# Kernel tuning notes

Hardware: AMD Instinct MI355X
Metric: run time of the kernel (lower is better)

## Reference

```python
import jax, jax.numpy as jnp
import numpy as np

NC = 128      # nc
K = 5         # cube kernel size
NS = 3        # n_scale pyramid levels
NV = 150000   # vertices (cortical-surface scale)
NF = 300000   # faces ~ 2*NV
L = 192       # volume side (L = W = H -> rescale = [1,1,1])


def setup_inputs() -> dict:
    key = jax.random.key(0)
    ks = jax.random.split(key, 16)
    s = 0.05
    return {
        "v": jax.random.uniform(ks[0], (1, NV, 3), minval=-0.9, maxval=0.9, dtype=jnp.float32),
        "f": jax.random.randint(ks[1], (1, NF, 3), 0, NV, dtype=jnp.int32),
        "volume": jax.random.normal(ks[2], (1, 1, L, L, L), dtype=jnp.float32),
        "fc1_w": jax.random.normal(ks[3], (6, NC), dtype=jnp.float32) * s,
        "fc1_b": jnp.zeros((NC,), jnp.float32),
        "fc2_w": jax.random.normal(ks[4], (2 * NC, 4 * NC), dtype=jnp.float32) * s,
        "fc2_b": jnp.zeros((4 * NC,), jnp.float32),
        "fc3_w": jax.random.normal(ks[5], (4 * NC, 2 * NC), dtype=jnp.float32) * s,
        "fc3_b": jnp.zeros((2 * NC,), jnp.float32),
        "fc4_w": jax.random.normal(ks[6], (2 * NC, 3), dtype=jnp.float32) * s,
        "fc4_b": jnp.zeros((3,), jnp.float32),
        "conv_w": jax.random.normal(ks[7], (NC, NS, K, K, K), dtype=jnp.float32) * s,
        "conv_b": jnp.zeros((NC,), jnp.float32),
        "lfc_w": jax.random.normal(ks[8], (NC, NC), dtype=jnp.float32) * s,
        "lfc_b": jnp.zeros((NC,), jnp.float32),
    }


def _vertex_normals(v, f):
    # pytorch3d-style vertex normals: scatter-add area-weighted face normals, then normalize.
    verts, faces = v[0], f[0]
    p0, p1, p2 = verts[faces[:, 0]], verts[faces[:, 1]], verts[faces[:, 2]]
    fn = jnp.cross(p1 - p0, p2 - p0)  # [NF, 3]
    n = jnp.zeros_like(verts)
    n = n.at[faces[:, 0]].add(fn).at[faces[:, 1]].add(fn).at[faces[:, 2]].add(fn)
    n = n / jnp.maximum(jnp.linalg.norm(n, axis=-1, keepdims=True), 1e-12)
    return n[None]  # [1, NV, 3]


def _cube_sampling(v, volume):
    # Vectorized version of the 125-iteration Python gather loop:
    # gather a KxKxK neighborhood per vertex at each pyramid scale.
    vol_n = volume[0, 0]
    off = jnp.arange(-(K - 1) // 2, (K - 1) // 2 + 1)  # [-2..2]
    cubes = []
    for n in range(NS):
        if n > 0:
            s = vol_n.shape[0]
            vol_n = vol_n.reshape(s // 2, 2, s // 2, 2, s // 2, 2).mean(axis=(1, 3, 5))  # avg_pool3d(2)
        idx = jnp.round((v[0] + 1.0) * L / 2 ** (n + 1)).astype(jnp.int32)  # rescale = [1,1,1]
        idx = jnp.clip(idx, (K - 1) // 2, L // 2 ** n - 3)
        i0 = idx[:, 0, None, None, None] + off[None, :, None, None]
        i1 = idx[:, 1, None, None, None] + off[None, None, :, None]
        i2 = idx[:, 2, None, None, None] + off[None, None, None, :]
        cubes.append(vol_n[i0, i1, i2])  # [NV, K, K, K]
    return jnp.stack(cubes, axis=1)  # [NV, NS, K, K, K]


def reference(v, f, volume, fc1_w, fc1_b, fc2_w, fc2_b, fc3_w, fc3_b, fc4_w, fc4_b,
              conv_w, conv_b, lfc_w, lfc_b):
    coord = v
    normal = _vertex_normals(v, f)
    x = jnp.concatenate([v, normal], axis=2)                 # [1, NV, 6]
    x = jax.nn.leaky_relu(x @ fc1_w + fc1_b, 0.15)           # [1, NV, NC]
    cubes = _cube_sampling(v, volume)                        # [NV, NS, K, K, K]
    # Conv3d with kernel == input size -> single output voxel == full contraction.
    x_local = jnp.einsum('ncijk,ocijk->no', cubes, conv_w) + conv_b  # [NV, NC]
    x_local = (x_local @ lfc_w + lfc_b)[None]                # [1, NV, NC]
    x = jnp.concatenate([x, x_local], axis=2)                # [1, NV, 2*NC]
    x = jax.nn.leaky_relu(x @ fc2_w + fc2_b, 0.15)
    x = jax.nn.leaky_relu(x @ fc3_w + fc3_b, 0.15)
    x = jnp.tanh(x @ fc4_w + fc4_b) * 0.1
    return coord + x
```

## Files before the change

kernel.cpp:

```cpp
#include <hip/hip_runtime.h>
#include <hip/hip_bf16.h>
#include <math.h>

#define NVERT 150000
#define NFACE 300000
#define LVOL  192
#define TVB   32
#define MTV   48

#define P2_POOL1 3456
#define P2_POOL2 432
#define P2_WC    193
#define P2_WC8   304
#define P2_CP0   3456
#define P2_POOL2_START (P2_POOL1)
#define P2_WC_START    (P2_POOL1 + P2_POOL2)
#define P2_WC8_START   (P2_WC_START + P2_WC)
#define P2_CP0_START   (P2_WC8_START + P2_WC8)

#define NB_NORM 1172
#define NB_TRS  1024

#define NBUCKET 13824
#define WS_BIG_NEED  44808576ull
#define WS_B16_NEED  58964352ull
#define WS_SORT_NEED 60219648ull

typedef short v8s __attribute__((ext_vector_type(8)));
typedef float v4f __attribute__((ext_vector_type(4)));
typedef unsigned int v4u __attribute__((ext_vector_type(4)));

__device__ __forceinline__ float s2f(short s) {
    unsigned int u = ((unsigned int)(unsigned short)s) << 16;
    return __builtin_bit_cast(float, u);
}
__device__ __forceinline__ short f2s(float f) {
    __hip_bfloat16 h = __float2bfloat16(f);
    return __builtin_bit_cast(short, h);
}
__device__ __forceinline__ float lrelu(float x) { return x > 0.f ? x : 0.15f * x; }

__device__ __forceinline__ float ldf(const void* __restrict__ p, int i, int bf) {
    return bf ? s2f(((const short*)p)[i]) : ((const float*)p)[i];
}

__device__ __forceinline__ int haddr(int r, int c) {
    int hi  = c >> 7;
    int mid = (c >> 4) & 7;
    int lo  = c & 15;
    int wc  = hi * 64 + (mid & 3) * 16 + lo;
    return ((mid < 4) ? 0 : 12672) + r * 264 + wc;
}

__global__ void detect_kernel(const void* __restrict__ v, int* __restrict__ flag) {
    __shared__ int s_ok;
    int t = threadIdx.x;
    if (t == 0) s_ok = 1;
    __syncthreads();
    float x = s2f(((const short*)v)[t]);
    if (!(fabsf(x) <= 1.0f)) atomicAnd(&s_ok, 0);
    __syncthreads();
    if (t == 0) *flag = s_ok;
}

__global__ __launch_bounds__(256) void sort_hist_kernel(
    const void* __restrict__ v, int* __restrict__ hist, int* __restrict__ keys,
    const int* __restrict__ flag)
{
    const int bf = *flag;
    int vert = blockIdx.x * 256 + threadIdx.x;
    if (vert >= NVERT) return;
    float vx = ldf(v, vert * 3 + 0, bf);
    float vy = ldf(v, vert * 3 + 1, bf);
    float vz = ldf(v, vert * 3 + 2, bf);
    int cx = min(max((int)rintf((vx + 1.0f) * 96.0f), 2), 189);
    int cy = min(max((int)rintf((vy + 1.0f) * 96.0f), 2), 189);
    int cz = min(max((int)rintf((vz + 1.0f) * 96.0f), 2), 189);
    int key = ((cx >> 3) * 24 + (cy >> 3)) * 24 + (cz >> 3);
    keys[vert] = key;
    atomicAdd(&hist[key], 1);
}

__global__ __launch_bounds__(1024) void sort_scan_kernel(int* __restrict__ hist)
{
    __shared__ int partial[1024];
    const int t = threadIdx.x;
    const int CH = 14;
    int base = t * CH;
    int sum = 0;
    #pragma unroll
    for (int i = 0; i < CH; i++) {
        int idx = base + i;
        if (idx < NBUCKET) sum += hist[idx];
    }
    partial[t] = sum;
    __syncthreads();
    for (int off = 1; off < 1024; off <<= 1) {
        int x = (t >= off) ? partial[t - off] : 0;
        __syncthreads();
        partial[t] += x;
        __syncthreads();
    }
    int run = partial[t] - sum;
    for (int i = 0; i < CH; i++) {
        int idx = base + i;
        if (idx < NBUCKET) {
            int c = hist[idx];
            hist[idx] = run;
            run += c;
        }
    }
}

__global__ __launch_bounds__(256) void sort_scatter_kernel(
    int* __restrict__ cursor, const int* __restrict__ keys, int* __restrict__ perm)
{
    int vert = blockIdx.x * 256 + threadIdx.x;
    if (vert >= NVERT) return;
    int pos = atomicAdd(&cursor[keys[vert]], 1);
    perm[pos] = vert;
}

__global__ __launch_bounds__(256) void mega_prep2_kernel(
    const void* __restrict__ volume,
    short* __restrict__ vol1b, short* __restrict__ vol2b,
    const void* __restrict__ conv_w, const void* __restrict__ lfc_w,
    const void* __restrict__ conv_b, const void* __restrict__ lfc_b,
    short* __restrict__ Wcomb, short* __restrict__ Wcomb8, float* __restrict__ bcomb,
    const int* __restrict__ flag,
    short* __restrict__ vol0b)
{
    const int bf = *flag;
    const int bid = blockIdx.x;
    const int t = threadIdx.x;

    if (bid < P2_POOL1) {
        int id = bid * 256 + t;
        int z = id % 96, y = (id / 96) % 96, x = id / (96 * 96);
        float s = 0.f;
        #pragma unroll
        for (int a = 0; a < 2; a++)
            #pragma unroll
            for (int b = 0; b < 2; b++)
                #pragma unroll
                for (int c = 0; c < 2; c++)
                    s += ldf(volume, (2 * x + a) * (LVOL * LVOL) + (2 * y + b) * LVOL + (2 * z + c), bf);
        s *= 0.125f;
        vol1b[id] = f2s(s);
    } else if (bid < P2_WC_START) {
        int id = (bid - P2_POOL2_START) * 256 + t;
        int z = id % 48, y = (id / 48) % 48, x = id / (48 * 48);
        float s = 0.f;
        for (int a = 0; a < 4; a++)
            for (int b = 0; b < 4; b++)
                #pragma unroll
                for (int c = 0; c < 4; c++)
                    s += ldf(volume, (4 * x + a) * (LVOL * LVOL) + (4 * y + b) * LVOL + (4 * z + c), bf);
        s *= 0.015625f;
        vol2b[id] = f2s(s);
    } else if (bid < P2_WC8_START) {
        int id = (bid - P2_WC_START) * 256 + t;
        if (id < 49152) {
            int j = id / 384, k = id - j * 384;
            float acc = 0.f;
            if (k < 375) {
                float a0 = 0.f, a1 = 0.f, a2 = 0.f, a3 = 0.f;
                for (int o = 0; o < 128; o += 4) {
                    a0 += ldf(conv_w, (o + 0) * 375 + k, bf) * ldf(lfc_w, (o + 0) * 128 + j, bf);
                    a1 += ldf(conv_w, (o + 1) * 375 + k, bf) * ldf(lfc_w, (o + 1) * 128 + j, bf);
                    a2 += ldf(conv_w, (o + 2) * 375 + k, bf) * ldf(lfc_w, (o + 2) * 128 + j, bf);
                    a3 += ldf(conv_w, (o + 3) * 375 + k, bf) * ldf(lfc_w, (o + 3) * 128 + j, bf);
                }
                acc = (a0 + a1) + (a2 + a3);
            }
            int tile = j >> 4, ln = j & 15;
            int kk = k >> 5, r = k & 31, qq = r >> 3, e = r & 7;
            Wcomb[((tile * 12 + kk) * 64 + qq * 16 + ln) * 8 + e] = f2s(acc);
        } else if (id < 49152 + 128) {
            int j = id - 49152;
            float acc = ldf(lfc_b, j, bf);
            for (int o = 0; o < 128; o++) acc += ldf(conv_b, o, bf) * ldf(lfc_w, o * 128 + j, bf);
            bcomb[j] = acc;
        }
    } else if (bid < P2_CP0_START) {
        int id = (bid - P2_WC8_START) * 256 + t;
        int j = id / 608, k = id - j * 608;
        int r = k >> 3, e = k & 7;
        float acc = 0.f;
        if (e < 5 && r < 75) {
            int k375 = (r / 25) * 125 + (r % 25) * 5 + e;
            float a0 = 0.f, a1 = 0.f, a2 = 0.f, a3 = 0.f;
            for (int o = 0; o < 128; o += 4) {
                a0 += ldf(conv_w, (o + 0) * 375 + k375, bf) * ldf(lfc_w, (o + 0) * 128 + j, bf);
                a1 += ldf(conv_w, (o + 1) * 375 + k375, bf) * ldf(lfc_w, (o + 1) * 128 + j, bf);
                a2 += ldf(conv_w, (o + 2) * 375 + k375, bf) * ldf(lfc_w, (o + 2) * 128 + j, bf);
                a3 += ldf(conv_w, (o + 3) * 375 + k375, bf) * ldf(lfc_w, (o + 3) * 128 + j, bf);
            }
            acc = (a0 + a1) + (a2 + a3);
        }
        int tile = j >> 4, ln = j & 15;
        int kk = k >> 5, rr = k & 31, qq = rr >> 3, ee = rr & 7;
        Wcomb8[((tile * 19 + kk) * 64 + qq * 16 + ln) * 8 + ee] = f2s(acc);
    } else {
        if (bf) return;
        int id = (bid - P2_CP0_START) * 2048 + t * 8;
        const float* vp = (const float*)volume;
        short tmp[8];
        #pragma unroll
        for (int i = 0; i < 8; i++) tmp[i] = f2s(vp[id + i]);
        *(v8s*)&vol0b[id] = *(v8s*)tmp;
    }
}

__global__ __launch_bounds__(256, 4) void gather8_kernel(
    const void* __restrict__ v,
    const int* __restrict__ f, float* __restrict__ n_accum,
    const void* __restrict__ volume,
    const short* __restrict__ vol1b,
    const short* __restrict__ vol2b,
    const short* __restrict__ vol0b,
    const int* __restrict__ perm,
    const short* __restrict__ Wcomb8,
    const float* __restrict__ bcomb,
    const void* __restrict__ fc2_w, const void* __restrict__ fc3_w,
    short* __restrict__ fc2T, short* __restrict__ fc3T,
    short* __restrict__ xloc,
    const int* __restrict__ flag, int ngather)
{
    __shared__ __align__(16) short sCube[TVB * 608];
    __shared__ int sIdx[TVB * 4];

    const int bf = *flag;
    const int t = threadIdx.x;
    const int bid = blockIdx.x;

    if (bid >= ngather) {
        int rb = bid - ngather;
        if (rb < NB_NORM) {
            int ft = rb * 256 + t;
            if (ft >= NFACE) return;
            int i0 = f[ft * 3 + 0], i1 = f[ft * 3 + 1], i2 = f[ft * 3 + 2];
            float p0x = ldf(v, i0 * 3 + 0, bf), p0y = ldf(v, i0 * 3 + 1, bf), p0z = ldf(v, i0 * 3 + 2, bf);
            float p1x = ldf(v, i1 * 3 + 0, bf), p1y = ldf(v, i1 * 3 + 1, bf), p1z = ldf(v, i1 * 3 + 2, bf);
            float p2x = ldf(v, i2 * 3 + 0, bf), p2y = ldf(v, i2 * 3 + 1, bf), p2z = ldf(v, i2 * 3 + 2, bf);
            float e1x = p1x - p0x, e1y = p1y - p0y, e1z = p1z - p0z;
            float e2x = p2x - p0x, e2y = p2y - p0y, e2z = p2z - p0z;
            float cx = e1y * e2z - e1z * e2y;
            float cy = e1z * e2x - e1x * e2z;
            float cz = e1x * e2y - e1y * e2x;
            atomicAdd(&n_accum[i0 * 3 + 0], cx); atomicAdd(&n_accum[i0 * 3 + 1], cy); atomicAdd(&n_accum[i0 * 3 + 2], cz);
            atomicAdd(&n_accum[i1 * 3 + 0], cx); atomicAdd(&n_accum[i1 * 3 + 1], cy); atomicAdd(&n_accum[i1 * 3 + 2], cz);
            atomicAdd(&n_accum[i2 * 3 + 0], cx); atomicAdd(&n_accum[i2 * 3 + 1], cy); atomicAdd(&n_accum[i2 * 3 + 2], cz);
        } else {
            int id = (rb - NB_NORM) * 256 + t;
            if (id < 131072) {
                int col = id >> 8, k = id & 255;
                int tile = col >> 4, ln = col & 15;
                int kk = k >> 5, r = k & 31, qq = r >> 3, e = r & 7;
                fc2T[((tile * 8 + kk) * 64 + qq * 16 + ln) * 8 + e] = f2s(ldf(fc2_w, k * 512 + col, bf));
            } else {
                int i = id - 131072;
                int col = i >> 9, k = i & 511;
                int tile = col >> 4, ln = col & 15;
                int kk = k >> 5, r = k & 31, qq = r >> 3, e = r & 7;
                fc3T[((tile * 16 + kk) * 64 + qq * 16 + ln) * 8 + e] = f2s(ldf(fc3_w, k * 256 + col, bf));
            }
        }
        return;
    }

    const int base = bid * TVB;
    const int w = t >> 6, L = t & 63, q = L >> 4, ln = L & 15;
    const short* v0 = bf ? (const short*)volume : vol0b;

    if (t < TVB) {
        int slot = min(base + t, NVERT - 1);
        int vert = perm ? perm[slot] : slot;
        float vx = ldf(v, vert * 3 + 0, bf);
        float vy = ldf(v, vert * 3 + 1, bf);
        float vz = ldf(v, vert * 3 + 2, bf);
        #pragma unroll
        for (int n = 0; n < 3; n++) {
            float scl = (n == 0) ? 96.0f : (n == 1 ? 48.0f : 24.0f);
            int dim = LVOL >> n, lim = dim - 3;
            int cx = min(max((int)rintf((vx + 1.0f) * scl), 2), lim);
            int cy = min(max((int)rintf((vy + 1.0f) * scl), 2), lim);
            int cz = min(max((int)rintf((vz + 1.0f) * scl), 2), lim);
            sIdx[t * 4 + n] = (cx * dim + cy) * dim + (cz - 2);
        }
        *(v4u*)&sCube[t * 608 + 600] = (v4u){0u, 0u, 0u, 0u};
    }
    __syncthreads();

    for (int idx = t; idx < TVB * 75; idx += 256) {
        int n   = idx / 800;
        int rem = idx - n * 800;
        int vl  = rem / 25;
        int dd  = rem - vl * 25;
        int di  = dd / 5, dj = dd - di * 5;
        int dim = LVOL >> n;
        int addr = sIdx[vl * 4 + n] + (di - 2) * dim * dim + (dj - 2) * dim;
        int r = n * 25 + dd;
        if (n == 0 && bf) {
            const short* vp = (const short*)volume;
            short* dst = &sCube[vl * 608 + r * 8];
            #pragma unroll
            for (int i = 0; i < 5; i++) dst[i] = vp[addr + i];
            dst[5] = 0; dst[6] = 0; dst[7] = 0;
        } else {
            const short* lvl = (n == 0) ? v0 : (n == 1 ? vol1b : vol2b);
            int p  = addr & 1;
            int a0 = addr - p;
            const unsigned int* u = (const unsigned int*)(lvl + a0);
            unsigned int x0 = u[0], x1 = u[1], x2 = u[2];
            unsigned int d0, d1, d2;
            if (p) {
                d0 = (x0 >> 16) | (x1 << 16);
                d1 = (x1 >> 16) | (x2 << 16);
                d2 = (x2 >> 16);
            } else {
                d0 = x0;
                d1 = x1;
                d2 = x2 & 0xFFFFu;
            }
            *(v4u*)&sCube[vl * 608 + r * 8] = (v4u){d0, d1, d2, 0u};
        }
    }
    __syncthreads();

    #pragma unroll
    for (int nt = 0; nt < 2; nt++) {
        int col = w * 32 + nt * 16 + ln;
        const short* wb = Wcomb8 + ((w * 2 + nt) * 19 * 64 + q * 16 + ln) * 8;
        v4f acc0 = {0.f, 0.f, 0.f, 0.f}, acc1 = {0.f, 0.f, 0.f, 0.f};
        #pragma unroll
        for (int k0 = 0; k0 < 19; k0++) {
            v8s b  = *(const v8s*)(wb + k0 * 512);
            v8s a0 = *(const v8s*)&sCube[ln * 608 + k0 * 32 + q * 8];
            v8s a1 = *(const v8s*)&sCube[(16 + ln) * 608 + k0 * 32 + q * 8];
            acc0 = __builtin_amdgcn_mfma_f32_16x16x32_bf16(a0, b, acc0, 0, 0, 0);
            acc1 = __builtin_amdgcn_mfma_f32_16x16x32_bf16(a1, b, acc1, 0, 0, 0);
        }
        float bias = bcomb[col];
        #pragma unroll
        for (int r = 0; r < 4; r++) {
            xloc[(base + q * 4 + r) * 128 + col]      = f2s(acc0[r] + bias);
            xloc[(base + 16 + q * 4 + r) * 128 + col] = f2s(acc1[r] + bias);
        }
    }
}

__global__ __launch_bounds__(256, 6) void gather_ext_kernel(
    const void* __restrict__ v,
    const int* __restrict__ f, float* __restrict__ n_accum,
    const void* __restrict__ volume,
    const short* __restrict__ vol1b,
    const short* __restrict__ vol2b,
    const short* __restrict__ vol0b,
    const int* __restrict__ perm,
    const short* __restrict__ Wcomb,
    const float* __restrict__ bcomb,
    const void* __restrict__ fc2_w, const void* __restrict__ fc3_w,
    short* __restrict__ fc2T, short* __restrict__ fc3T,
    short* __restrict__ xloc,
    const int* __restrict__ flag, int ngather)
{
    __shared__ __align__(16) short sCube[TVB * 392];
    __shared__ int sIdx[TVB * 4];

    const int bf = *flag;
    const int t = threadIdx.x;
    const int bid = blockIdx.x;

    if (bid >= ngather) {
        int rb = bid - ngather;
        if (rb < NB_NORM) {
            int ft = rb * 256 + t;
            if (ft >= NFACE) return;
            int i0 = f[ft * 3 + 0], i1 = f[ft * 3 + 1], i2 = f[ft * 3 + 2];
            float p0x = ldf(v, i0 * 3 + 0, bf), p0y = ldf(v, i0 * 3 + 1, bf), p0z = ldf(v, i0 * 3 + 2, bf);
            float p1x = ldf(v, i1 * 3 + 0, bf), p1y = ldf(v, i1 * 3 + 1, bf), p1z = ldf(v, i1 * 3 + 2, bf);
            float p2x = ldf(v, i2 * 3 + 0, bf), p2y = ldf(v, i2 * 3 + 1, bf), p2z = ldf(v, i2 * 3 + 2, bf);
            float e1x = p1x - p0x, e1y = p1y - p0y, e1z = p1z - p0z;
            float e2x = p2x - p0x, e2y = p2y - p0y, e2z = p2z - p0z;
            float cx = e1y * e2z - e1z * e2y;
            float cy = e1z * e2x - e1x * e2z;
            float cz = e1x * e2y - e1y * e2x;
            atomicAdd(&n_accum[i0 * 3 + 0], cx); atomicAdd(&n_accum[i0 * 3 + 1], cy); atomicAdd(&n_accum[i0 * 3 + 2], cz);
            atomicAdd(&n_accum[i1 * 3 + 0], cx); atomicAdd(&n_accum[i1 * 3 + 1], cy); atomicAdd(&n_accum[i1 * 3 + 2], cz);
            atomicAdd(&n_accum[i2 * 3 + 0], cx); atomicAdd(&n_accum[i2 * 3 + 1], cy); atomicAdd(&n_accum[i2 * 3 + 2], cz);
        } else {
            int id = (rb - NB_NORM) * 256 + t;
            if (id < 131072) {
                int col = id >> 8, k = id & 255;
                int tile = col >> 4, ln = col & 15;
                int kk = k >> 5, r = k & 31, qq = r >> 3, e = r & 7;
                fc2T[((tile * 8 + kk) * 64 + qq * 16 + ln) * 8 + e] = f2s(ldf(fc2_w, k * 512 + col, bf));
            } else {
                int i = id - 131072;
                int col = i >> 9, k = i & 511;
                int tile = col >> 4, ln = col & 15;
                int kk = k >> 5, r = k & 31, qq = r >> 3, e = r & 7;
                fc3T[((tile * 16 + kk) * 64 + qq * 16 + ln) * 8 + e] = f2s(ldf(fc3_w, k * 256 + col, bf));
            }
        }
        return;
    }

    const int base = bid * TVB;
    const int w = t >> 6, L = t & 63, q = L >> 4, ln = L & 15;
    const short* v0 = bf ? (const short*)volume : vol0b;

    if (t < TVB) {
        int slot = min(base + t, NVERT - 1);
        int vert = perm ? perm[slot] : slot;
        float vx = ldf(v, vert * 3 + 0, bf);
        float vy = ldf(v, vert * 3 + 1, bf);
        float vz = ldf(v, vert * 3 + 2, bf);
        #pragma unroll
        for (int n = 0; n < 3; n++) {
            float scl = (n == 0) ? 96.0f : (n == 1 ? 48.0f : 24.0f);
            int dim = LVOL >> n, lim = dim - 3;
            int cx = min(max((int)rintf((vx + 1.0f) * scl), 2), lim);
            int cy = min(max((int)rintf((vy + 1.0f) * scl), 2), lim);
            int cz = min(max((int)rintf((vz + 1.0f) * scl), 2), lim);
            sIdx[t * 4 + n] = (cx * dim + cy) * dim + (cz - 2);
        }
    }
    __syncthreads();

    for (int idx = t; idx < TVB * 75; idx += 256) {
        int n   = idx / 800;
        int rem = idx - n * 800;
        int vl  = rem / 25;
        int dd  = rem - vl * 25;
        int di  = dd / 5, dj = dd - di * 5;
        int dim = LVOL >> n;
        int addr = sIdx[vl * 4 + n] + (di - 2) * dim * dim + (dj - 2) * dim;
        short* dst = &sCube[vl * 392 + n * 125 + dd * 5];
        if (n == 0 && v0 == nullptr) {
            const float* vp = (const float*)volume;
            #pragma unroll
            for (int i = 0; i < 5; i++) dst[i] = f2s(vp[addr + i]);
        } else {
            const short* lvl = (n == 0) ? v0 : (n == 1 ? vol1b : vol2b);
            #pragma unroll
            for (int i = 0; i < 5; i++) dst[i] = lvl[addr + i];
        }
    }
    for (int idx = t; idx < TVB * 9; idx += 256) {
        int vl = idx / 9, rr = idx - vl * 9;
        sCube[vl * 392 + 375 + rr] = 0;
    }
    __syncthreads();

    #pragma unroll
    for (int nt = 0; nt < 2; nt++) {
        int col = w * 32 + nt * 16 + ln;
        const short* wb = Wcomb + ((w * 2 + nt) * 12 * 64 + q * 16 + ln) * 8;
        v4f acc0 = {0.f, 0.f, 0.f, 0.f}, acc1 = {0.f, 0.f, 0.f, 0.f};
        #pragma unroll
        for (int k0 = 0; k0 < 12; k0++) {
            v8s b  = *(const v8s*)(wb + k0 * 512);
            v8s a0 = *(const v8s*)&sCube[ln * 392 + k0 * 32 + q * 8];
            v8s a1 = *(const v8s*)&sCube[(16 + ln) * 392 + k0 * 32 + q * 8];
            acc0 = __builtin_amdgcn_mfma_f32_16x16x32_bf16(a0, b, acc0, 0, 0, 0);
            acc1 = __builtin_amdgcn_mfma_f32_16x16x32_bf16(a1, b, acc1, 0, 0, 0);
        }
        float bias = bcomb[col];
        #pragma unroll
        for (int r = 0; r < 4; r++) {
            xloc[(base + q * 4 + r) * 128 + col]      = f2s(acc0[r] + bias);
            xloc[(base + 16 + q * 4 + r) * 128 + col] = f2s(acc1[r] + bias);
        }
    }
}

__global__ __launch_bounds__(256, 3) void mlp_kernel(
    const void* __restrict__ v,
    const float* __restrict__ n_accum,
    const short* __restrict__ xloc,
    const int* __restrict__ perm,
    const short* __restrict__ fc2T,
    const short* __restrict__ fc3T,
    const void* __restrict__ fc1_w, const void* __restrict__ fc1_b,
    const void* __restrict__ fc2_b, const void* __restrict__ fc3_b,
    const void* __restrict__ fc4_w, const void* __restrict__ fc4_b,
    void* __restrict__ out,
    const int* __restrict__ flag)
{
    __shared__ __align__(16) char smem[52224];
    short* sX  = (short*)smem;
    short* sHB = (short*)smem;
    short* s3  = (short*)smem;
    short* sW4 = (short*)(smem + 50688);

    const int bf = *flag;
    const int t = threadIdx.x;
    const int base = blockIdx.x * MTV;
    const int w = t >> 6, L = t & 63, q = L >> 4, ln = L & 15;
    const int laneoff = (q * 16 + ln) * 8;

    for (int id = t; id < MTV * 16; id += 256) {
        int row = id >> 4, seg = id & 15;
        v8s x = *(const v8s*)(xloc + (base + row) * 128 + seg * 8);
        *(v8s*)&sX[row * 264 + 128 + seg * 8] = x;
    }

    for (int i = t; i < 768; i += 256) {
        int j = i >> 8, k = i & 255;
        sW4[i] = f2s(ldf(fc4_w, k * 3 + j, bf));
    }

    {
        int vi = t >> 2, cb = (t & 3) * 32;
        if (vi < MTV) {
            int vert = perm ? perm[base + vi] : (base + vi);
            float i0 = ldf(v, vert * 3 + 0, bf);
            float i1 = ldf(v, vert * 3 + 1, bf);
            float i2 = ldf(v, vert * 3 + 2, bf);
            float nx = n_accum[vert * 3 + 0];
            float ny = n_accum[vert * 3 + 1];
            float nz = n_accum[vert * 3 + 2];
            float inv = 1.0f / fmaxf(sqrtf(nx * nx + ny * ny + nz * nz), 1e-12f);
            float i3 = nx * inv, i4 = ny * inv, i5 = nz * inv;
            #pragma unroll 8
            for (int i = 0; i < 32; i++) {
                int c = cb + i;
                float acc = ldf(fc1_b, c, bf)
                          + i0 * ldf(fc1_w, 0 * 128 + c, bf)
                          + i1 * ldf(fc1_w, 1 * 128 + c, bf)
                          + i2 * ldf(fc1_w, 2 * 128 + c, bf)
                          + i3 * ldf(fc1_w, 3 * 128 + c, bf)
                          + i4 * ldf(fc1_w, 4 * 128 + c, bf)
                          + i5 * ldf(fc1_w, 5 * 128 + c, bf);
                sX[vi * 264 + c] = f2s(lrelu(acc));
            }
        }
    }
    __syncthreads();

    {
        #pragma unroll
        for (int nt = 4; nt < 8; nt++) {
            int col = w * 128 + nt * 16 + ln;
            const short* bb = fc2T + (w * 8 + nt) * 8 * 512 + laneoff;
            v4f acc0 = {0.f, 0.f, 0.f, 0.f}, acc1 = {0.f, 0.f, 0.f, 0.f}, acc2 = {0.f, 0.f, 0.f, 0.f};
            #pragma unroll
            for (int k0 = 0; k0 < 8; k0++) {
                v8s b  = *(const v8s*)(bb + k0 * 512);
                v8s a0 = *(const v8s*)&sX[(ln) * 264 + k0 * 32 + q * 8];
                v8s a1 = *(const v8s*)&sX[(16 + ln) * 264 + k0 * 32 + q * 8];
                v8s a2 = *(const v8s*)&sX[(32 + ln) * 264 + k0 * 32 + q * 8];
                acc0 = __builtin_amdgcn_mfma_f32_16x16x32_bf16(a0, b, acc0, 0, 0, 0);
                acc1 = __builtin_amdgcn_mfma_f32_16x16x32_bf16(a1, b, acc1, 0, 0, 0);
                acc2 = __builtin_amdgcn_mfma_f32_16x16x32_bf16(a2, b, acc2, 0, 0, 0);
            }
            float bias = ldf(fc2_b, col, bf);
            int wc = 12672 + w * 64 + (nt - 4) * 16 + ln;
            #pragma unroll
            for (int r = 0; r < 4; r++) {
                sHB[(q * 4 + r) * 264 + wc]      = f2s(lrelu(acc0[r] + bias));
                sHB[(16 + q * 4 + r) * 264 + wc] = f2s(lrelu(acc1[r] + bias));
                sHB[(32 + q * 4 + r) * 264 + wc] = f2s(lrelu(acc2[r] + bias));
            }
        }

        v4f accL[4][3];
        #pragma unroll
        for (int nt = 0; nt < 4; nt++)
            #pragma unroll
            for (int m = 0; m < 3; m++)
                accL[nt][m] = (v4f){0.f, 0.f, 0.f, 0.f};

        #pragma unroll
        for (int nt = 0; nt < 4; nt++) {
            const short* bb = fc2T + (w * 8 + nt) * 8 * 512 + laneoff;
            #pragma unroll
            for (int k0 = 0; k0 < 8; k0++) {
                v8s b  = *(const v8s*)(bb + k0 * 512);
                v8s a0 = *(const v8s*)&sX[(ln) * 264 + k0 * 32 + q * 8];
                v8s a1 = *(const v8s*)&sX[(16 + ln) * 264 + k0 * 32 + q * 8];
                v8s a2 = *(const v8s*)&sX[(32 + ln) * 264 + k0 * 32 + q * 8];
                accL[nt][0] = __builtin_amdgcn_mfma_f32_16x16x32_bf16(a0, b, accL[nt][0], 0, 0, 0);
                accL[nt][1] = __builtin_amdgcn_mfma_f32_16x16x32_bf16(a1, b, accL[nt][1], 0, 0, 0);
                accL[nt][2] = __builtin_amdgcn_mfma_f32_16x16x32_bf16(a2, b, accL[nt][2], 0, 0, 0);
            }
        }
        __syncthreads();

        #pragma unroll
        for (int nt = 0; nt < 4; nt++) {
            int col = w * 128 + nt * 16 + ln;
            float bias = ldf(fc2_b, col, bf);
            int wc = w * 64 + nt * 16 + ln;
            #pragma unroll
            for (int r = 0; r < 4; r++) {
                sHB[(q * 4 + r) * 264 + wc]      = f2s(lrelu(accL[nt][0][r] + bias));
                sHB[(16 + q * 4 + r) * 264 + wc] = f2s(lrelu(accL[nt][1][r] + bias));
                sHB[(32 + q * 4 + r) * 264 + wc] = f2s(lrelu(accL[nt][2][r] + bias));
            }
        }
    }
    __syncthreads();

    {
        v4f acc[4][3];
        #pragma unroll
        for (int nt = 0; nt < 4; nt++)
            #pragma unroll
            for (int m = 0; m < 3; m++)
                acc[nt][m] = (v4f){0.f, 0.f, 0.f, 0.f};

        #pragma unroll
        for (int half = 0; half < 2; half++) {
            v8s A0[8], A1[8], A2[8];
            #pragma unroll
            for (int k0 = 0; k0 < 8; k0++) {
                int c = half * 256 + k0 * 32 + q * 8;
                A0[k0] = *(const v8s*)&sHB[haddr(ln, c)];
                A1[k0] = *(const v8s*)&sHB[haddr(16 + ln, c)];
                A2[k0] = *(const v8s*)&sHB[haddr(32 + ln, c)];
            }
            #pragma unroll
            for (int nt = 0; nt < 4; nt++) {
                const short* bb = fc3T + ((w * 4 + nt) * 16 + half * 8) * 512 + laneoff;
                v8s B[8];
                #pragma unroll
                for (int k0 = 0; k0 < 8; k0++) B[k0] = *(const v8s*)(bb + k0 * 512);
                #pragma unroll
                for (int k0 = 0; k0 < 8; k0++) {
                    acc[nt][0] = __builtin_amdgcn_mfma_f32_16x16x32_bf16(A0[k0], B[k0], acc[nt][0], 0, 0, 0);
                    acc[nt][1] = __builtin_amdgcn_mfma_f32_16x16x32_bf16(A1[k0], B[k0], acc[nt][1], 0, 0, 0);
                    acc[nt][2] = __builtin_amdgcn_mfma_f32_16x16x32_bf16(A2[k0], B[k0], acc[nt][2], 0, 0, 0);
                }
            }
        }
        __syncthreads();

        #pragma unroll
        for (int nt = 0; nt < 4; nt++) {
            int col = w * 64 + nt * 16 + ln;
            float bias = ldf(fc3_b, col, bf);
            #pragma unroll
            for (int r = 0; r < 4; r++) {
                s3[(q * 4 + r) * 264 + col]      = f2s(lrelu(acc[nt][0][r] + bias));
                s3[(16 + q * 4 + r) * 264 + col] = f2s(lrelu(acc[nt][1][r] + bias));
                s3[(32 + q * 4 + r) * 264 + col] = f2s(lrelu(acc[nt][2][r] + bias));
            }
        }
    }
    __syncthreads();

    {
        int vi = t >> 2, l = t & 3;
        if (vi < MTV) {
            float p0 = 0.f, p1 = 0.f, p2 = 0.f;
            for (int k = l * 8; k < 256; k += 32) {
                #pragma unroll
                for (int j = 0; j < 8; j++) {
                    float a = s2f(s3[vi * 264 + k + j]);
                    p0 += a * s2f(sW4[0 * 256 + k + j]);
                    p1 += a * s2f(sW4[1 * 256 + k + j]);
                    p2 += a * s2f(sW4[2 * 256 + k + j]);
                }
            }
            #pragma unroll
            for (int s = 2; s; s >>= 1) {
                p0 += __shfl_down(p0, s, 4);
                p1 += __shfl_down(p1, s, 4);
                p2 += __shfl_down(p2, s, 4);
            }
            if (l == 0) {
                int vert = perm ? perm[base + vi] : (base + vi);
                float vx = ldf(v, vert * 3 + 0, bf);
                float vy = ldf(v, vert * 3 + 1, bf);
                float vz = ldf(v, vert * 3 + 2, bf);
                float o0 = vx + 0.1f * tanhf(p0 + ldf(fc4_b, 0, bf));
                float o1 = vy + 0.1f * tanhf(p1 + ldf(fc4_b, 1, bf));
                float o2 = vz + 0.1f * tanhf(p2 + ldf(fc4_b, 2, bf));
                if (bf) {
                    short* ob = (short*)out;
                    ob[vert * 3 + 0] = f2s(o0);
                    ob[vert * 3 + 1] = f2s(o1);
                    ob[vert * 3 + 2] = f2s(o2);
                } else {
                    float* of = (float*)out;
                    of[vert * 3 + 0] = o0;
                    of[vert * 3 + 1] = o1;
                    of[vert * 3 + 2] = o2;
                }
            }
        }
    }
}

__global__ __launch_bounds__(256, 3) void fused_mfma_kernel(
    const void* __restrict__ v,
    const float* __restrict__ n_accum,
    const void* __restrict__ volume,
    const short* __restrict__ vol1,
    const short* __restrict__ vol2,
    const short* __restrict__ Wcomb,
    const float* __restrict__ bcomb,
    const short* __restrict__ fc2T,
    const short* __restrict__ fc3T,
    const void* __restrict__ fc1_w, const void* __restrict__ fc1_b,
    const void* __restrict__ fc2_b, const void* __restrict__ fc3_b,
    const void* __restrict__ fc4_w, const void* __restrict__ fc4_b,
    void* __restrict__ out,
    const int* __restrict__ flag)
{
    __shared__ __align__(16) char smem[51712];
    short* sX    = (short*)smem;
    short* sCube = (short*)(smem + 16896);
    short* sH    = (short*)(smem + 16896);
    short* s3    = (short*)smem;
    short* sW4   = (short*)(smem + 50176);

    const int bf = *flag;
    const int t = threadIdx.x;
    const int base = blockIdx.x * TVB;
    const int w = t >> 6, L = t & 63, q = L >> 4, ln = L & 15;
    const int laneoff = (q * 16 + ln) * 8;

    for (int idx = t; idx < TVB * 75; idx += 256) {
        int vl  = idx / 75;
        int r75 = idx - vl * 75;
        int n   = r75 / 25;
        int dd  = r75 - n * 25;
        int di  = dd / 5, dj = dd - di * 5;
        int vert = base + vl;
        short* dst = &sCube[vl * 392 + n * 125 + dd * 5];
        if (vert < NVERT) {
            float vx = ldf(v, vert * 3 + 0, bf);
            float vy = ldf(v, vert * 3 + 1, bf);
            float vz = ldf(v, vert * 3 + 2, bf);
            float scl = (n == 0) ? 96.0f : (n == 1 ? 48.0f : 24.0f);
            int lim = (LVOL >> n) - 3;
            int cx = (int)rintf((vx + 1.0f) * scl);
            int cy = (int)rintf((vy + 1.0f) * scl);
            int cz = (int)rintf((vz + 1.0f) * scl);
            cx = min(max(cx, 2), lim) + di - 2;
            cy = min(max(cy, 2), lim) + dj - 2;
            cz = min(max(cz, 2), lim);
            if (n == 0) {
                int b0 = (cx * LVOL + cy) * LVOL + (cz - 2);
                if (bf) {
                    const short* vp = (const short*)volume;
                    #pragma unroll
                    for (int i = 0; i < 5; i++) dst[i] = vp[b0 + i];
                } else {
                    const float* vp = (const float*)volume;
                    #pragma unroll
                    for (int i = 0; i < 5; i++) dst[i] = f2s(vp[b0 + i]);
                }
            } else {
                const short* lvl = (n == 1) ? vol1 : vol2;
                int dim = (n == 1) ? 96 : 48;
                int b0 = (cx * dim + cy) * dim + (cz - 2);
// ... 118 lines not shown
        }
    }
    __syncthreads();

    {
        int vi = t >> 3, l = t & 7;
        float p0 = 0.f, p1 = 0.f, p2 = 0.f;
        for (int k = l; k < 256; k += 8) {
            float a = s2f(s3[vi * 264 + k]);
            p0 += a * s2f(sW4[0 * 256 + k]);
            p1 += a * s2f(sW4[1 * 256 + k]);
            p2 += a * s2f(sW4[2 * 256 + k]);
        }
        #pragma unroll
        for (int s = 4; s; s >>= 1) {
            p0 += __shfl_down(p0, s, 8);
            p1 += __shfl_down(p1, s, 8);
            p2 += __shfl_down(p2, s, 8);
        }
        if (l == 0) {
            int vert = base + vi;
            if (vert < NVERT) {
                float vx = ldf(v, vert * 3 + 0, bf);
                float vy = ldf(v, vert * 3 + 1, bf);
                float vz = ldf(v, vert * 3 + 2, bf);
                float o0 = vx + 0.1f * tanhf(p0 + ldf(fc4_b, 0, bf));
                float o1 = vy + 0.1f * tanhf(p1 + ldf(fc4_b, 1, bf));
                float o2 = vz + 0.1f * tanhf(p2 + ldf(fc4_b, 2, bf));
                if (bf) {
                    short* ob = (short*)out;
                    ob[vert * 3 + 0] = f2s(o0);
                    ob[vert * 3 + 1] = f2s(o1);
                    ob[vert * 3 + 2] = f2s(o2);
                } else {
                    float* of = (float*)out;
                    of[vert * 3 + 0] = o0;
                    of[vert * 3 + 1] = o1;
                    of[vert * 3 + 2] = o2;
                }
            }
        }
    }
}

extern "C" void kernel_launch(void* const* d_in, const int* in_sizes, int n_in,
                              void* d_out, int out_size, void* d_ws, size_t ws_size,
                              hipStream_t stream) {
    const void* v      = d_in[0];
    const int*  f      = (const int*)d_in[1];
    const void* volume = d_in[2];
    const void* fc1_w  = d_in[3];
    const void* fc1_b  = d_in[4];
    const void* fc2_w  = d_in[5];
    const void* fc2_b  = d_in[6];
    const void* fc3_w  = d_in[7];
    const void* fc3_b  = d_in[8];
    const void* fc4_w  = d_in[9];
    const void* fc4_b  = d_in[10];
    const void* conv_w = d_in[11];
    const void* conv_b = d_in[12];
    const void* lfc_w  = d_in[13];
    const void* lfc_b  = d_in[14];

    char* wsb = (char*)d_ws;
    const int big  = (ws_size >= WS_BIG_NEED) ? 1 : 0;
    const int b16  = (ws_size >= WS_B16_NEED) ? 1 : 0;
    const int srt  = (ws_size >= WS_SORT_NEED) ? 1 : 0;

    if (big) {
        int*   flag    = (int*)wsb;
        float* n_accum = (float*)(wsb + 64);
        short* vol1b   = (short*)(wsb + 1800064);
        short* vol2b   = (short*)(wsb + 5339008);
        short* Wcomb8  = (short*)(wsb + 5560192);
        short* Wcomb   = (short*)(wsb + 5781376);
        float* bcomb   = (float*)(wsb + 5879680);
        short* fc2T    = (short*)(wsb + 5880192);
        short* fc3T    = (short*)(wsb + 6142336);
        short* xloc    = (short*)(wsb + 6404480);
        short* vol0b   = b16 ? (short*)(wsb + 44808576) : nullptr;
        int*   hist    = srt ? (int*)(wsb + 58964352) : nullptr;
        int*   keys    = srt ? (int*)(wsb + 59019648) : nullptr;
        int*   perm    = srt ? (int*)(wsb + 59619648) : nullptr;

        hipMemsetAsync(n_accum, 0, NVERT * 3 * sizeof(float), stream);
        detect_kernel<<<1, 256, 0, stream>>>(v, flag);
        if (srt) {
            hipMemsetAsync(hist, 0, NBUCKET * sizeof(int), stream);
            sort_hist_kernel<<<(NVERT + 255) / 256, 256, 0, stream>>>(v, hist, keys, flag);
            sort_scan_kernel<<<1, 1024, 0, stream>>>(hist);
            sort_scatter_kernel<<<(NVERT + 255) / 256, 256, 0, stream>>>(hist, keys, perm);
        }
        mega_prep2_kernel<<<P2_CP0_START + (b16 ? P2_CP0 : 0), 256, 0, stream>>>(
            volume, vol1b, vol2b,
            conv_w, lfc_w, conv_b, lfc_b, Wcomb, Wcomb8, bcomb, flag, vol0b);
        int ngather = (NVERT + TVB - 1) / TVB;
        if (srt) {
            gather8_kernel<<<ngather + NB_NORM + NB_TRS, 256, 0, stream>>>(
                v, f, n_accum, volume, vol1b, vol2b, vol0b, perm, Wcomb8, bcomb,
                fc2_w, fc3_w, fc2T, fc3T, xloc, flag, ngather);
        } else {
            gather_ext_kernel<<<ngather + NB_NORM + NB_TRS, 256, 0, stream>>>(
                v, f, n_accum, volume, vol1b, vol2b, vol0b, nullptr, Wcomb, bcomb,
                fc2_w, fc3_w, fc2T, fc3T, xloc, flag, ngather);
        }
        mlp_kernel<<<(NVERT + MTV - 1) / MTV, 256, 0, stream>>>(
            v, n_accum, xloc, perm, fc2T, fc3T,
            fc1_w, fc1_b, fc2_b, fc3_b, fc4_w, fc4_b, d_out, flag);
    } else {
        int*   flag    = (int*)wsb;
        float* n_accum = (float*)(wsb + 64);
        short* vol1    = (short*)(wsb + 1800064);
        short* vol2    = (short*)(wsb + 3569536);
        short* Wcomb   = (short*)(wsb + 3790720);
        float* bcomb   = (float*)(wsb + 3889024);
        short* fc2T    = (short*)(wsb + 3889536);
        short* fc3T    = (short*)(wsb + 4151680);

        hipMemsetAsync(n_accum, 0, NVERT * 3 * sizeof(float), stream);
        detect_kernel<<<1, 256, 0, stream>>>(v, flag);
        mega_prep2_kernel<<<P2_WC8_START, 256, 0, stream>>>(
            volume, vol1, vol2,
            conv_w, lfc_w, conv_b, lfc_b, Wcomb, nullptr, bcomb, flag, nullptr);
        gather_ext_kernel<<<NB_NORM + NB_TRS, 256, 0, stream>>>(
            v, f, n_accum, volume, vol1, vol2, nullptr, nullptr, Wcomb, bcomb,
            fc2_w, fc3_w, fc2T, fc3T, nullptr, flag, 0);
        fused_mfma_kernel<<<(NVERT + TVB - 1) / TVB, 256, 0, stream>>>(
            v, n_accum, volume, vol1, vol2, Wcomb, bcomb, fc2T, fc3T,
            fc1_w, fc1_b, fc2_b, fc3_b, fc4_w, fc4_b, d_out, flag);
    }
}
```

Baseline: 550.6 us.

## Store sorted vertex coords and rank-indexed normals to avoid perm indirection

The sort scatter step now also writes each vertex's sorted position and a copy of its coordinates in sorted order. Face-normal atomics accumulate into the sorted slot via the rank array. The gather and MLP kernels can then read coordinates and normals contiguously by slot instead of going through perm. This removes scattered indirect loads in the hot kernels at the cost of extra workspace, an extra rank lookup per face vertex, and extra writes in the scatter kernel.

```diff
diff --git a/kernel.cpp b/kernel.cpp
--- a/kernel.cpp
+++ b/kernel.cpp
@@ -24,7 +24,7 @@
 #define NBUCKET 13824
 #define WS_BIG_NEED  44808576ull
 #define WS_B16_NEED  58964352ull
-#define WS_SORT_NEED 60219648ull
+#define WS_SORT_NEED 62619648ull
 
 typedef short v8s __attribute__((ext_vector_type(8)));
 typedef float v4f __attribute__((ext_vector_type(4)));
@@ -113,12 +113,20 @@
 }
 
 __global__ __launch_bounds__(256) void sort_scatter_kernel(
-    int* __restrict__ cursor, const int* __restrict__ keys, int* __restrict__ perm)
+    const void* __restrict__ v,
+    int* __restrict__ cursor, const int* __restrict__ keys,
+    int* __restrict__ perm, int* __restrict__ rank, float* __restrict__ vperm,
+    const int* __restrict__ flag)
 {
+    const int bf = *flag;
     int vert = blockIdx.x * 256 + threadIdx.x;
     if (vert >= NVERT) return;
     int pos = atomicAdd(&cursor[keys[vert]], 1);
     perm[pos] = vert;
+    rank[vert] = pos;
+    vperm[pos * 3 + 0] = ldf(v, vert * 3 + 0, bf);
+    vperm[pos * 3 + 1] = ldf(v, vert * 3 + 1, bf);
+    vperm[pos * 3 + 2] = ldf(v, vert * 3 + 2, bf);
 }
 
 __global__ __launch_bounds__(256) void mega_prep2_kernel(
@@ -219,7 +227,8 @@
     const short* __restrict__ vol1b,
     const short* __restrict__ vol2b,
     const short* __restrict__ vol0b,
-    const int* __restrict__ perm,
+    const float* __restrict__ vperm,
+    const int* __restrict__ rank,
     const short* __restrict__ Wcomb8,
     const float* __restrict__ bcomb,
     const void* __restrict__ fc2_w, const void* __restrict__ fc3_w,
@@ -228,6 +237,143 @@
     const int* __restrict__ flag, int ngather)
 {
     __shared__ __align__(16) short sCube[TVB * 608];
+    __shared__ int sIdx[TVB * 4];
+
+    const int bf = *flag;
+    const int t = threadIdx.x;
+    const int bid = blockIdx.x;
+
+    if (bid >= ngather) {
+        int rb = bid - ngather;
+        if (rb < NB_NORM) {
+            int ft = rb * 256 + t;
+            if (ft >= NFACE) return;
+            int i0 = f[ft * 3 + 0], i1 = f[ft * 3 + 1], i2 = f[ft * 3 + 2];
+            float p0x = ldf(v, i0 * 3 + 0, bf), p0y = ldf(v, i0 * 3 + 1, bf), p0z = ldf(v, i0 * 3 + 2, bf);
+            float p1x = ldf(v, i1 * 3 + 0, bf), p1y = ldf(v, i1 * 3 + 1, bf), p1z = ldf(v, i1 * 3 + 2, bf);
+            float p2x = ldf(v, i2 * 3 + 0, bf), p2y = ldf(v, i2 * 3 + 1, bf), p2z = ldf(v, i2 * 3 + 2, bf);
+            float e1x = p1x - p0x, e1y = p1y - p0y, e1z = p1z - p0z;
+            float e2x = p2x - p0x, e2y = p2y - p0y, e2z = p2z - p0z;
+            float cx = e1y * e2z - e1z * e2y;
+            float cy = e1z * e2x - e1x * e2z;
+            float cz = e1x * e2y - e1y * e2x;
+            int s0 = rank[i0], s1 = rank[i1], s2 = rank[i2];
+            atomicAdd(&n_accum[s0 * 3 + 0], cx); atomicAdd(&n_accum[s0 * 3 + 1], cy); atomicAdd(&n_accum[s0 * 3 + 2], cz);
+            atomicAdd(&n_accum[s1 * 3 + 0], cx); atomicAdd(&n_accum[s1 * 3 + 1], cy); atomicAdd(&n_accum[s1 * 3 + 2], cz);
+            atomicAdd(&n_accum[s2 * 3 + 0], cx); atomicAdd(&n_accum[s2 * 3 + 1], cy); atomicAdd(&n_accum[s2 * 3 + 2], cz);
+        } else {
+            int id = (rb - NB_NORM) * 256 + t;
+            if (id < 131072) {
+                int col = id >> 8, k = id & 255;
+                int tile = col >> 4, ln = col & 15;
+                int kk = k >> 5, r = k & 31, qq = r >> 3, e = r & 7;
+                fc2T[((tile * 8 + kk) * 64 + qq * 16 + ln) * 8 + e] = f2s(ldf(fc2_w, k * 512 + col, bf));
+            } else {
+                int i = id - 131072;
+                int col = i >> 9, k = i & 511;
+                int tile = col >> 4, ln = col & 15;
+                int kk = k >> 5, r = k & 31, qq = r >> 3, e = r & 7;
+                fc3T[((tile * 16 + kk) * 64 + qq * 16 + ln) * 8 + e] = f2s(ldf(fc3_w, k * 256 + col, bf));
+            }
+        }
+        return;
+    }
+
+    const int base = bid * TVB;
+    const int w = t >> 6, L = t & 63, q = L >> 4, ln = L & 15;
+    const short* v0 = bf ? (const short*)volume : vol0b;
+
+    if (t < TVB) {
+        int slot = min(base + t, NVERT - 1);
+        float vx = vperm[slot * 3 + 0];
+        float vy = vperm[slot * 3 + 1];
+        float vz = vperm[slot * 3 + 2];
+        #pragma unroll
+        for (int n = 0; n < 3; n++) {
+            float scl = (n == 0) ? 96.0f : (n == 1 ? 48.0f : 24.0f);
+            int dim = LVOL >> n, lim = dim - 3;
+            int cx = min(max((int)rintf((vx + 1.0f) * scl), 2), lim);
+            int cy = min(max((int)rintf((vy + 1.0f) * scl), 2), lim);
+            int cz = min(max((int)rintf((vz + 1.0f) * scl), 2), lim);
+            sIdx[t * 4 + n] = (cx * dim + cy) * dim + (cz - 2);
+        }
+        *(v4u*)&sCube[t * 608 + 600] = (v4u){0u, 0u, 0u, 0u};
+    }
+    __syncthreads();
+
+    for (int idx = t; idx < TVB * 75; idx += 256) {
+        int n   = idx / 800;
+        int rem = idx - n * 800;
+        int vl  = rem / 25;
+        int dd  = rem - vl * 25;
+        int di  = dd / 5, dj = dd - di * 5;
+        int dim = LVOL >> n;
+        int addr = sIdx[vl * 4 + n] + (di - 2) * dim * dim + (dj - 2) * dim;
+        int r = n * 25 + dd;
+        if (n == 0 && bf) {
+            const short* vp = (const short*)volume;
+            short* dst = &sCube[vl * 608 + r * 8];
+            #pragma unroll
+            for (int i = 0; i < 5; i++) dst[i] = vp[addr + i];
+            dst[5] = 0; dst[6] = 0; dst[7] = 0;
+        } else {
+            const short* lvl = (n == 0) ? v0 : (n == 1 ? vol1b : vol2b);
+            int p  = addr & 1;
+            int a0 = addr - p;
+            const unsigned int* u = (const unsigned int*)(lvl + a0);
+            unsigned int x0 = u[0], x1 = u[1], x2 = u[2];
+            unsigned int d0, d1, d2;
+            if (p) {
+                d0 = (x0 >> 16) | (x1 << 16);
+                d1 = (x1 >> 16) | (x2 << 16);
+                d2 = (x2 >> 16);
+            } else {
+                d0 = x0;
+                d1 = x1;
+                d2 = x2 & 0xFFFFu;
+            }
+            *(v4u*)&sCube[vl * 608 + r * 8] = (v4u){d0, d1, d2, 0u};
+        }
+    }
+    __syncthreads();
+
+    #pragma unroll
+    for (int nt = 0; nt < 2; nt++) {
+        int col = w * 32 + nt * 16 + ln;
+        const short* wb = Wcomb8 + ((w * 2 + nt) * 19 * 64 + q * 16 + ln) * 8;
+        v4f acc0 = {0.f, 0.f, 0.f, 0.f}, acc1 = {0.f, 0.f, 0.f, 0.f};
+        #pragma unroll
+        for (int k0 = 0; k0 < 19; k0++) {
+            v8s b  = *(const v8s*)(wb + k0 * 512);
+            v8s a0 = *(const v8s*)&sCube[ln * 608 + k0 * 32 + q * 8];
+            v8s a1 = *(const v8s*)&sCube[(16 + ln) * 608 + k0 * 32 + q * 8];
+            acc0 = __builtin_amdgcn_mfma_f32_16x16x32_bf16(a0, b, acc0, 0, 0, 0);
+            acc1 = __builtin_amdgcn_mfma_f32_16x16x32_bf16(a1, b, acc1, 0, 0, 0);
+        }
+        float bias = bcomb[col];
+        #pragma unroll
+        for (int r = 0; r < 4; r++) {
+            xloc[(base + q * 4 + r) * 128 + col]      = f2s(acc0[r] + bias);
+            xloc[(base + 16 + q * 4 + r) * 128 + col] = f2s(acc1[r] + bias);
+        }
+    }
+}
+
+__global__ __launch_bounds__(256, 6) void gather_ext_kernel(
+    const void* __restrict__ v,
+    const int* __restrict__ f, float* __restrict__ n_accum,
+    const void* __restrict__ volume,
+    const short* __restrict__ vol1b,
+    const short* __restrict__ vol2b,
+    const short* __restrict__ vol0b,
+    const short* __restrict__ Wcomb,
+    const float* __restrict__ bcomb,
+    const void* __restrict__ fc2_w, const void* __restrict__ fc3_w,
+    short* __restrict__ fc2T, short* __restrict__ fc3T,
+    short* __restrict__ xloc,
+    const int* __restrict__ flag, int ngather)
+{
+    __shared__ __align__(16) short sCube[TVB * 392];
     __shared__ int sIdx[TVB * 4];
 
     const int bf = *flag;
@@ -274,146 +420,7 @@
     const short* v0 = bf ? (const short*)volume : vol0b;
 
     if (t < TVB) {
-        int slot = min(base + t, NVERT - 1);
-        int vert = perm ? perm[slot] : slot;
-        float vx = ldf(v, vert * 3 + 0, bf);
-        float vy = ldf(v, vert * 3 + 1, bf);
-        float vz = ldf(v, vert * 3 + 2, bf);
-        #pragma unroll
-        for (int n = 0; n < 3; n++) {
-            float scl = (n == 0) ? 96.0f : (n == 1 ? 48.0f : 24.0f);
-            int dim = LVOL >> n, lim = dim - 3;
-            int cx = min(max((int)rintf((vx + 1.0f) * scl), 2), lim);
-            int cy = min(max((int)rintf((vy + 1.0f) * scl), 2), lim);
-            int cz = min(max((int)rintf((vz + 1.0f) * scl), 2), lim);
-            sIdx[t * 4 + n] = (cx * dim + cy) * dim + (cz - 2);
-        }
-        *(v4u*)&sCube[t * 608 + 600] = (v4u){0u, 0u, 0u, 0u};
-    }
-    __syncthreads();
-
-    for (int idx = t; idx < TVB * 75; idx += 256) {
-        int n   = idx / 800;
-        int rem = idx - n * 800;
-        int vl  = rem / 25;
-        int dd  = rem - vl * 25;
-        int di  = dd / 5, dj = dd - di * 5;
-        int dim = LVOL >> n;
-        int addr = sIdx[vl * 4 + n] + (di - 2) * dim * dim + (dj - 2) * dim;
-        int r = n * 25 + dd;
-        if (n == 0 && bf) {
-            const short* vp = (const short*)volume;
-            short* dst = &sCube[vl * 608 + r * 8];
-            #pragma unroll
-            for (int i = 0; i < 5; i++) dst[i] = vp[addr + i];
-            dst[5] = 0; dst[6] = 0; dst[7] = 0;
-        } else {
-            const short* lvl = (n == 0) ? v0 : (n == 1 ? vol1b : vol2b);
-            int p  = addr & 1;
-            int a0 = addr - p;
-            const unsigned int* u = (const unsigned int*)(lvl + a0);
-            unsigned int x0 = u[0], x1 = u[1], x2 = u[2];
-            unsigned int d0, d1, d2;
-            if (p) {
-                d0 = (x0 >> 16) | (x1 << 16);
-                d1 = (x1 >> 16) | (x2 << 16);
-                d2 = (x2 >> 16);
-            } else {
-                d0 = x0;
-                d1 = x1;
-                d2 = x2 & 0xFFFFu;
-            }
-            *(v4u*)&sCube[vl * 608 + r * 8] = (v4u){d0, d1, d2, 0u};
-        }
-    }
-    __syncthreads();
-
-    #pragma unroll
-    for (int nt = 0; nt < 2; nt++) {
-        int col = w * 32 + nt * 16 + ln;
-        const short* wb = Wcomb8 + ((w * 2 + nt) * 19 * 64 + q * 16 + ln) * 8;
-        v4f acc0 = {0.f, 0.f, 0.f, 0.f}, acc1 = {0.f, 0.f, 0.f, 0.f};
-        #pragma unroll
-        for (int k0 = 0; k0 < 19; k0++) {
-            v8s b  = *(const v8s*)(wb + k0 * 512);
-            v8s a0 = *(const v8s*)&sCube[ln * 608 + k0 * 32 + q * 8];
-            v8s a1 = *(const v8s*)&sCube[(16 + ln) * 608 + k0 * 32 + q * 8];
-            acc0 = __builtin_amdgcn_mfma_f32_16x16x32_bf16(a0, b, acc0, 0, 0, 0);
-            acc1 = __builtin_amdgcn_mfma_f32_16x16x32_bf16(a1, b, acc1, 0, 0, 0);
-        }
-        float bias = bcomb[col];
-        #pragma unroll
-        for (int r = 0; r < 4; r++) {
-            xloc[(base + q * 4 + r) * 128 + col]      = f2s(acc0[r] + bias);
-            xloc[(base + 16 + q * 4 + r) * 128 + col] = f2s(acc1[r] + bias);
-        }
-    }
-}
-
-__global__ __launch_bounds__(256, 6) void gather_ext_kernel(
-    const void* __restrict__ v,
-    const int* __restrict__ f, float* __restrict__ n_accum,
-    const void* __restrict__ volume,
-    const short* __restrict__ vol1b,
-    const short* __restrict__ vol2b,
-    const short* __restrict__ vol0b,
-    const int* __restrict__ perm,
-    const short* __restrict__ Wcomb,
-    const float* __restrict__ bcomb,
-    const void* __restrict__ fc2_w, const void* __restrict__ fc3_w,
-    short* __restrict__ fc2T, short* __restrict__ fc3T,
-    short* __restrict__ xloc,
-    const int* __restrict__ flag, int ngather)
-{
-    __shared__ __align__(16) short sCube[TVB * 392];
-    __shared__ int sIdx[TVB * 4];
-
-    const int bf = *flag;
-    const int t = threadIdx.x;
-    const int bid = blockIdx.x;
-
-    if (bid >= ngather) {
-        int rb = bid - ngather;
-        if (rb < NB_NORM) {
-            int ft = rb * 256 + t;
-            if (ft >= NFACE) return;
-            int i0 = f[ft * 3 + 0], i1 = f[ft * 3 + 1], i2 = f[ft * 3 + 2];
-            float p0x = ldf(v, i0 * 3 + 0, bf), p0y = ldf(v, i0 * 3 + 1, bf), p0z = ldf(v, i0 * 3 + 2, bf);
-            float p1x = ldf(v, i1 * 3 + 0, bf), p1y = ldf(v, i1 * 3 + 1, bf), p1z = ldf(v, i1 * 3 + 2, bf);
-            float p2x = ldf(v, i2 * 3 + 0, bf), p2y = ldf(v, i2 * 3 + 1, bf), p2z = ldf(v, i2 * 3 + 2, bf);
-            float e1x = p1x - p0x, e1y = p1y - p0y, e1z = p1z - p0z;
-            float e2x = p2x - p0x, e2y = p2y - p0y, e2z = p2z - p0z;
-            float cx = e1y * e2z - e1z * e2y;
-            float cy = e1z * e2x - e1x * e2z;
-            float cz = e1x * e2y - e1y * e2x;
-            atomicAdd(&n_accum[i0 * 3 + 0], cx); atomicAdd(&n_accum[i0 * 3 + 1], cy); atomicAdd(&n_accum[i0 * 3 + 2], cz);
-            atomicAdd(&n_accum[i1 * 3 + 0], cx); atomicAdd(&n_accum[i1 * 3 + 1], cy); atomicAdd(&n_accum[i1 * 3 + 2], cz);
-            atomicAdd(&n_accum[i2 * 3 + 0], cx); atomicAdd(&n_accum[i2 * 3 + 1], cy); atomicAdd(&n_accum[i2 * 3 + 2], cz);
-        } else {
-            int id = (rb - NB_NORM) * 256 + t;
-            if (id < 131072) {
-                int col = id >> 8, k = id & 255;
-                int tile = col >> 4, ln = col & 15;
-                int kk = k >> 5, r = k & 31, qq = r >> 3, e = r & 7;
-                fc2T[((tile * 8 + kk) * 64 + qq * 16 + ln) * 8 + e] = f2s(ldf(fc2_w, k * 512 + col, bf));
-            } else {
-                int i = id - 131072;
-                int col = i >> 9, k = i & 511;
-                int tile = col >> 4, ln = col & 15;
-                int kk = k >> 5, r = k & 31, qq = r >> 3, e = r & 7;
-                fc3T[((tile * 16 + kk) * 64 + qq * 16 + ln) * 8 + e] = f2s(ldf(fc3_w, k * 256 + col, bf));
-            }
-        }
-        return;
-    }
-
-    const int base = bid * TVB;
-    const int w = t >> 6, L = t & 63, q = L >> 4, ln = L & 15;
-    const short* v0 = bf ? (const short*)volume : vol0b;
-
-    if (t < TVB) {
-        int slot = min(base + t, NVERT - 1);
-        int vert = perm ? perm[slot] : slot;
+        int vert = min(base + t, NVERT - 1);
         float vx = ldf(v, vert * 3 + 0, bf);
         float vy = ldf(v, vert * 3 + 1, bf);
         float vz = ldf(v, vert * 3 + 2, bf);
@@ -478,6 +485,7 @@
 
 __global__ __launch_bounds__(256, 3) void mlp_kernel(
     const void* __restrict__ v,
+    const float* __restrict__ vperm,
     const float* __restrict__ n_accum,
     const short* __restrict__ xloc,
     const int* __restrict__ perm,
@@ -515,13 +523,20 @@
     {
         int vi = t >> 2, cb = (t & 3) * 32;
         if (vi < MTV) {
-            int vert = perm ? perm[base + vi] : (base + vi);
-            float i0 = ldf(v, vert * 3 + 0, bf);
-            float i1 = ldf(v, vert * 3 + 1, bf);
-            float i2 = ldf(v, vert * 3 + 2, bf);
-            float nx = n_accum[vert * 3 + 0];
-            float ny = n_accum[vert * 3 + 1];
-            float nz = n_accum[vert * 3 + 2];
+            int slot = base + vi;
+            float i0, i1, i2;
+            if (vperm) {
+                i0 = vperm[slot * 3 + 0];
+                i1 = vperm[slot * 3 + 1];
+                i2 = vperm[slot * 3 + 2];
+            } else {
+                i0 = ldf(v, slot * 3 + 0, bf);
+                i1 = ldf(v, slot * 3 + 1, bf);
+                i2 = ldf(v, slot * 3 + 2, bf);
+            }
+            float nx = n_accum[slot * 3 + 0];
+            float ny = n_accum[slot * 3 + 1];
+            float nz = n_accum[slot * 3 + 2];
             float inv = 1.0f / fmaxf(sqrtf(nx * nx + ny * ny + nz * nz), 1e-12f);
             float i3 = nx * inv, i4 = ny * inv, i5 = nz * inv;
             #pragma unroll 8
@@ -672,10 +687,18 @@
                 p2 += __shfl_down(p2, s, 4);
             }
             if (l == 0) {
-                int vert = perm ? perm[base + vi] : (base + vi);
-                float vx = ldf(v, vert * 3 + 0, bf);
-                float vy = ldf(v, vert * 3 + 1, bf);
-                float vz = ldf(v, vert * 3 + 2, bf);
+                int slot = base + vi;
+                int vert = perm ? perm[slot] : slot;
+                float vx, vy, vz;
+                if (vperm) {
+                    vx = vperm[slot * 3 + 0];
+                    vy = vperm[slot * 3 + 1];
+                    vz = vperm[slot * 3 + 2];
+                } else {
+                    vx = ldf(v, slot * 3 + 0, bf);
+                    vy = ldf(v, slot * 3 + 1, bf);
+                    vz = ldf(v, slot * 3 + 2, bf);
+                }
                 float o0 = vx + 0.1f * tanhf(p0 + ldf(fc4_b, 0, bf));
                 float o1 = vy + 0.1f * tanhf(p1 + ldf(fc4_b, 1, bf));
                 float o2 = vz + 0.1f * tanhf(p2 + ldf(fc4_b, 2, bf));
@@ -960,6 +983,8 @@
         int*   hist    = srt ? (int*)(wsb + 58964352) : nullptr;
         int*   keys    = srt ? (int*)(wsb + 59019648) : nullptr;
         int*   perm    = srt ? (int*)(wsb + 59619648) : nullptr;
+        int*   rank    = srt ? (int*)(wsb + 60219648) : nullptr;
+        float* vperm   = srt ? (float*)(wsb + 60819648) : nullptr;
 
         hipMemsetAsync(n_accum, 0, NVERT * 3 * sizeof(float), stream);
         detect_kernel<<<1, 256, 0, stream>>>(v, flag);
@@ -967,7 +992,7 @@
             hipMemsetAsync(hist, 0, NBUCKET * sizeof(int), stream);
             sort_hist_kernel<<<(NVERT + 255) / 256, 256, 0, stream>>>(v, hist, keys, flag);
             sort_scan_kernel<<<1, 1024, 0, stream>>>(hist);
-            sort_scatter_kernel<<<(NVERT + 255) / 256, 256, 0, stream>>>(hist, keys, perm);
+            sort_scatter_kernel<<<(NVERT + 255) / 256, 256, 0, stream>>>(v, hist, keys, perm, rank, vperm, flag);
         }
         mega_prep2_kernel<<<P2_CP0_START + (b16 ? P2_CP0 : 0), 256, 0, stream>>>(
             volume, vol1b, vol2b,
@@ -975,15 +1000,15 @@
         int ngather = (NVERT + TVB - 1) / TVB;
         if (srt) {
             gather8_kernel<<<ngather + NB_NORM + NB_TRS, 256, 0, stream>>>(
-                v, f, n_accum, volume, vol1b, vol2b, vol0b, perm, Wcomb8, bcomb,
+                v, f, n_accum, volume, vol1b, vol2b, vol0b, vperm, rank, Wcomb8, bcomb,
                 fc2_w, fc3_w, fc2T, fc3T, xloc, flag, ngather);
         } else {
             gather_ext_kernel<<<ngather + NB_NORM + NB_TRS, 256, 0, stream>>>(
-                v, f, n_accum, volume, vol1b, vol2b, vol0b, nullptr, Wcomb, bcomb,
+                v, f, n_accum, volume, vol1b, vol2b, vol0b, Wcomb, bcomb,
                 fc2_w, fc3_w, fc2T, fc3T, xloc, flag, ngather);
         }
         mlp_kernel<<<(NVERT + MTV - 1) / MTV, 256, 0, stream>>>(
-            v, n_accum, xloc, perm, fc2T, fc3T,
+            v, vperm, n_accum, xloc, perm, fc2T, fc3T,
             fc1_w, fc1_b, fc2_b, fc3_b, fc4_w, fc4_b, d_out, flag);
     } else {
         int*   flag    = (int*)wsb;
@@ -1001,7 +1026,7 @@
             volume, vol1, vol2,
             conv_w, lfc_w, conv_b, lfc_b, Wcomb, nullptr, bcomb, flag, nullptr);
         gather_ext_kernel<<<NB_NORM + NB_TRS, 256, 0, stream>>>(
-            v, f, n_accum, volume, vol1, vol2, nullptr, nullptr, Wcomb, bcomb,
+            v, f, n_accum, volume, vol1, vol2, nullptr, Wcomb, bcomb,
             fc2_w, fc3_w, fc2T, fc3T, nullptr, flag, 0);
         fused_mfma_kernel<<<(NVERT + TVB - 1) / TVB, 256, 0, stream>>>(
             v, n_accum, volume, vol1, vol2, Wcomb, bcomb, fc2T, fc3T,
```

Measured after the change: 528.2 us. 4.1% less time.
